# Kernel optimization log

Measured on AMD Instinct MI355X. Metric: run time of the kernel, lower is better.

Reference implementation:

```python
import jax, jax.numpy as jnp
import numpy as np

NU = 0.5

def _conv3x3(x, w):
    # x: [B,1,Hp,Wp] padded, w: [1,1,3,3]; VALID conv -> [B,1,H,W]
    return jax.lax.conv_general_dilated(
        x, w, window_strides=(1, 1), padding='VALID',
        dimension_numbers=('NCHW', 'OIHW', 'NCHW'))


def setup_inputs() -> dict:
    key = jax.random.key(0)
    k1, k2, k3, k4, k5 = jax.random.split(key, 5)
    B, H, W = 16, 1024, 1024
    u = jax.random.normal(k1, (B, 1, H, W), dtype=jnp.float32)
    u_vel = jax.random.normal(k2, (B, 1, H, W), dtype=jnp.float32)
    w1 = jax.random.normal(k3, (1, 1, 3, 3), dtype=jnp.float32)
    w2 = jax.random.normal(k4, (1, 1, 3, 3), dtype=jnp.float32)
    w3 = jax.random.normal(k5, (1, 1, 3, 3), dtype=jnp.float32)
    return {"u": u, "u_vel": u_vel, "w1": w1, "w2": w2, "w3": w3}


def reference(u, u_vel, w1, w2, w3):
    # replicate pad by 1 on H and W (torch 'replicate' == numpy 'edge')
    u_pad = jnp.pad(u, ((0, 0), (0, 0), (1, 1), (1, 1)), mode='edge')
    Lu = NU * _conv3x3(u_pad, w1) - u_vel * _conv3x3(u_pad, w2) - u_vel * _conv3x3(u_pad, w3)
    return Lu
```

## Files before the change

kernel.cpp:

```cpp
#include <hip/hip_runtime.h>


#define HH 1024
#define WW 1024
#define RPB 4
#define PPT 4
#define TPB (WW / PPT)

__device__ __forceinline__ float rfl(float x) {
    union { float f; int i; } c; c.f = x;
    c.i = __builtin_amdgcn_readfirstlane(c.i);
    return c.f;
}

__global__ __launch_bounds__(TPB) void burgers_stencil(
    const float* __restrict__ u,
    const float* __restrict__ uvel,
    const float* __restrict__ w1,
    const float* __restrict__ w2,
    const float* __restrict__ w3,
    float* __restrict__ out,
    int rowBlocks)
{
    const int tid = threadIdx.x;
    const int b   = blockIdx.x / rowBlocks;
    const int y0  = (blockIdx.x % rowBlocks) * RPB;
    const int x0  = tid * PPT;

    const size_t img = (size_t)b * HH * WW;
    const float* ub  = u + img;

    const int xl = (x0 == 0) ? 0 : x0 - 1;
    const int xr = (x0 + PPT >= WW) ? WW - 1 : x0 + PPT;

    float4 uv[RPB + 2]; float ul[RPB + 2], ur[RPB + 2];
#pragma unroll
    for (int i = 0; i < RPB + 2; ++i) {
        int yr = y0 - 1 + i;
        yr = yr < 0 ? 0 : (yr > HH - 1 ? HH - 1 : yr);
        const float* row = ub + (size_t)yr * WW;
        uv[i] = *(const float4*)(row + x0);
        ul[i] = row[xl];
        ur[i] = row[xr];
    }
    float4 vv[RPB];
#pragma unroll
    for (int r = 0; r < RPB; ++r)
        vv[r] = *(const float4*)(uvel + img + (size_t)(y0 + r) * WW + x0);

    float W1[9], W23[9];
#pragma unroll
    for (int i = 0; i < 9; ++i) {
        W1[i]  = rfl(w1[i]);
        W23[i] = rfl(w2[i] + w3[i]);
    }

    __builtin_amdgcn_sched_barrier(0);

#pragma unroll
    for (int r = 0; r < RPB; ++r) {
        float p[3][PPT + 2];
#pragma unroll
        for (int rr = 0; rr < 3; ++rr) {
            const int i = r + rr;
            p[rr][0] = ul[i];
            p[rr][1] = uv[i].x; p[rr][2] = uv[i].y;
            p[rr][3] = uv[i].z; p[rr][4] = uv[i].w;
            p[rr][5] = ur[i];
        }
        const float vel[PPT] = {vv[r].x, vv[r].y, vv[r].z, vv[r].w};

        float o[PPT];
#pragma unroll
        for (int j = 0; j < PPT; ++j) {
            float c1 = 0.f, c23 = 0.f;
#pragma unroll
            for (int rr = 0; rr < 3; ++rr) {
#pragma unroll
                for (int k = 0; k < 3; ++k) {
                    const float a = p[rr][j + k];
                    c1  = fmaf(W1[rr*3 + k],  a, c1);
                    c23 = fmaf(W23[rr*3 + k], a, c23);
                }
            }
            o[j] = 0.5f * c1 - vel[j] * c23;
        }
        float4 ov; ov.x = o[0]; ov.y = o[1]; ov.z = o[2]; ov.w = o[3];
        *(float4*)(out + img + (size_t)(y0 + r) * WW + x0) = ov;
    }
}

extern "C" void kernel_launch(void* const* d_in, const int* in_sizes, int n_in,
                              void* d_out, int out_size, void* d_ws, size_t ws_size,
                              hipStream_t stream) {
    const float* u    = (const float*)d_in[0];
    const float* uvel = (const float*)d_in[1];
    const float* w1   = (const float*)d_in[2];
    const float* w2   = (const float*)d_in[3];
    const float* w3   = (const float*)d_in[4];
    float* out        = (float*)d_out;

    const int B = in_sizes[0] / (HH * WW);
    const int rowBlocks = HH / RPB;
    dim3 grid(B * rowBlocks);
    dim3 block(TPB);
    burgers_stencil<<<grid, block, 0, stream>>>(u, uvel, w1, w2, w3, out, rowBlocks);
}
```

Measured before the change: 179.0 us.

## Stage stencil input rows into LDS via direct global-to-LDS loads

Measured after the change: 174.5 us. 1.03x faster.

```diff
diff --git a/kernel.cpp b/kernel.cpp
--- a/kernel.cpp
+++ b/kernel.cpp
@@ -4,8 +4,11 @@
 #define HH 1024
 #define WW 1024
 #define RPB 4
-#define PPT 4
-#define TPB (WW / PPT)
+#define TPB 256
+#define NROW (RPB + 2)
+
+typedef __attribute__((address_space(3))) void       lds_void;
+typedef __attribute__((address_space(1))) const void gbl_void;
 
 __device__ __forceinline__ float rfl(float x) {
     union { float f; int i; } c; c.f = x;
@@ -22,27 +25,28 @@
     float* __restrict__ out,
     int rowBlocks)
 {
-    const int tid = threadIdx.x;
-    const int b   = blockIdx.x / rowBlocks;
-    const int y0  = (blockIdx.x % rowBlocks) * RPB;
-    const int x0  = tid * PPT;
+    __shared__ float tile[NROW * WW];
+
+    const int tid  = threadIdx.x;
+    const int wave = tid >> 6;
+    const int lane = tid & 63;
+    const int b    = blockIdx.x / rowBlocks;
+    const int y0   = (blockIdx.x % rowBlocks) * RPB;
+    const int x0   = tid * 4;
 
     const size_t img = (size_t)b * HH * WW;
     const float* ub  = u + img;
 
-    const int xl = (x0 == 0) ? 0 : x0 - 1;
-    const int xr = (x0 + PPT >= WW) ? WW - 1 : x0 + PPT;
-
-    float4 uv[RPB + 2]; float ul[RPB + 2], ur[RPB + 2];
 #pragma unroll
-    for (int i = 0; i < RPB + 2; ++i) {
+    for (int i = 0; i < NROW; ++i) {
         int yr = y0 - 1 + i;
         yr = yr < 0 ? 0 : (yr > HH - 1 ? HH - 1 : yr);
-        const float* row = ub + (size_t)yr * WW;
-        uv[i] = *(const float4*)(row + x0);
-        ul[i] = row[xl];
-        ur[i] = row[xr];
+        const float* g = ub + (size_t)yr * WW + wave * 256 + lane * 4;
+        __builtin_amdgcn_global_load_lds((gbl_void*)g,
+                                         (lds_void*)&tile[i * WW + wave * 256],
+                                         16, 0, 0);
     }
+
     float4 vv[RPB];
 #pragma unroll
     for (int r = 0; r < RPB; ++r)
@@ -55,24 +59,28 @@
         W23[i] = rfl(w2[i] + w3[i]);
     }
 
-    __builtin_amdgcn_sched_barrier(0);
+    __syncthreads();
+
+    const int xm1 = (x0 == 0)       ? 0      : x0 - 1;
+    const int xp4 = (x0 + 4 >= WW)  ? WW - 1 : x0 + 4;
 
 #pragma unroll
     for (int r = 0; r < RPB; ++r) {
-        float p[3][PPT + 2];
+        float p[3][6];
 #pragma unroll
         for (int rr = 0; rr < 3; ++rr) {
-            const int i = r + rr;
-            p[rr][0] = ul[i];
-            p[rr][1] = uv[i].x; p[rr][2] = uv[i].y;
-            p[rr][3] = uv[i].z; p[rr][4] = uv[i].w;
-            p[rr][5] = ur[i];
+            const float* row = &tile[(r + rr) * WW];
+            const float4 m = *(const float4*)(row + x0);
+            p[rr][0] = row[xm1];
+            p[rr][1] = m.x; p[rr][2] = m.y;
+            p[rr][3] = m.z; p[rr][4] = m.w;
+            p[rr][5] = row[xp4];
         }
-        const float vel[PPT] = {vv[r].x, vv[r].y, vv[r].z, vv[r].w};
+        const float vel[4] = {vv[r].x, vv[r].y, vv[r].z, vv[r].w};
 
-        float o[PPT];
+        float o[4];
 #pragma unroll
-        for (int j = 0; j < PPT; ++j) {
+        for (int j = 0; j < 4; ++j) {
             float c1 = 0.f, c23 = 0.f;
 #pragma unroll
             for (int rr = 0; rr < 3; ++rr) {
```

## Use single-wave blocks covering 8 rows by 256 columns with waves-per-EU hint

Applied to the files above, without the earlier changes.

After: 174.3 us. -2.6%, faster.

```diff
diff --git a/kernel.cpp b/kernel.cpp
--- a/kernel.cpp
+++ b/kernel.cpp
@@ -3,9 +3,9 @@
 
 #define HH 1024
 #define WW 1024
-#define RPB 4
-#define PPT 4
-#define TPB (WW / PPT)
+#define RPB 8
+#define CPW 256
+#define NROW (RPB + 2)
 
 __device__ __forceinline__ float rfl(float x) {
     union { float f; int i; } c; c.f = x;
@@ -13,29 +13,42 @@
     return c.f;
 }
 
-__global__ __launch_bounds__(TPB) void burgers_stencil(
+__global__ __attribute__((amdgpu_flat_work_group_size(64, 64),
+                          amdgpu_waves_per_eu(1, 2)))
+void burgers_stencil(
     const float* __restrict__ u,
     const float* __restrict__ uvel,
     const float* __restrict__ w1,
     const float* __restrict__ w2,
     const float* __restrict__ w3,
     float* __restrict__ out,
-    int rowBlocks)
+    int rowBlocks, int colBlocks)
 {
-    const int tid = threadIdx.x;
-    const int b   = blockIdx.x / rowBlocks;
-    const int y0  = (blockIdx.x % rowBlocks) * RPB;
-    const int x0  = tid * PPT;
+    const int lane = threadIdx.x;
+    int rem = blockIdx.x;
+    const int xb = rem % colBlocks; rem /= colBlocks;
+    const int yb = rem % rowBlocks; rem /= rowBlocks;
+    const int b  = rem;
+
+    const int y0 = yb * RPB;
+    const int x0 = xb * CPW + lane * 4;
 
     const size_t img = (size_t)b * HH * WW;
     const float* ub  = u + img;
 
+    float W1[9], W23[9];
+#pragma unroll
+    for (int i = 0; i < 9; ++i) {
+        W1[i]  = rfl(w1[i]);
+        W23[i] = rfl(w2[i] + w3[i]);
+    }
+
     const int xl = (x0 == 0) ? 0 : x0 - 1;
-    const int xr = (x0 + PPT >= WW) ? WW - 1 : x0 + PPT;
+    const int xr = (x0 + 4 >= WW) ? WW - 1 : x0 + 4;
 
-    float4 uv[RPB + 2]; float ul[RPB + 2], ur[RPB + 2];
+    float4 uv[NROW]; float ul[NROW], ur[NROW];
 #pragma unroll
-    for (int i = 0; i < RPB + 2; ++i) {
+    for (int i = 0; i < NROW; ++i) {
         int yr = y0 - 1 + i;
         yr = yr < 0 ? 0 : (yr > HH - 1 ? HH - 1 : yr);
         const float* row = ub + (size_t)yr * WW;
@@ -48,18 +61,11 @@
     for (int r = 0; r < RPB; ++r)
         vv[r] = *(const float4*)(uvel + img + (size_t)(y0 + r) * WW + x0);
 
-    float W1[9], W23[9];
-#pragma unroll
-    for (int i = 0; i < 9; ++i) {
-        W1[i]  = rfl(w1[i]);
-        W23[i] = rfl(w2[i] + w3[i]);
-    }
-
     __builtin_amdgcn_sched_barrier(0);
 
 #pragma unroll
     for (int r = 0; r < RPB; ++r) {
-        float p[3][PPT + 2];
+        float p[3][6];
 #pragma unroll
         for (int rr = 0; rr < 3; ++rr) {
             const int i = r + rr;
@@ -68,11 +74,11 @@
             p[rr][3] = uv[i].z; p[rr][4] = uv[i].w;
             p[rr][5] = ur[i];
         }
-        const float vel[PPT] = {vv[r].x, vv[r].y, vv[r].z, vv[r].w};
+        const float vel[4] = {vv[r].x, vv[r].y, vv[r].z, vv[r].w};
 
-        float o[PPT];
+        float o[4];
 #pragma unroll
-        for (int j = 0; j < PPT; ++j) {
+        for (int j = 0; j < 4; ++j) {
             float c1 = 0.f, c23 = 0.f;
 #pragma unroll
             for (int rr = 0; rr < 3; ++rr) {
@@ -83,7 +89,7 @@
                     c23 = fmaf(W23[rr*3 + k], a, c23);
                 }
             }
-            o[j] = 0.5f * c1 - vel[j] * c23;
+            o[j] = fmaf(-vel[j], c23, 0.5f * c1);
         }
         float4 ov; ov.x = o[0]; ov.y = o[1]; ov.z = o[2]; ov.w = o[3];
         *(float4*)(out + img + (size_t)(y0 + r) * WW + x0) = ov;
@@ -102,7 +108,9 @@
 
     const int B = in_sizes[0] / (HH * WW);
     const int rowBlocks = HH / RPB;
-    dim3 grid(B * rowBlocks);
-    dim3 block(TPB);
-    burgers_stencil<<<grid, block, 0, stream>>>(u, uvel, w1, w2, w3, out, rowBlocks);
+    const int colBlocks = WW / CPW;
+    dim3 grid(B * rowBlocks * colBlocks);
+    dim3 block(64);
+    burgers_stencil<<<grid, block, 0, stream>>>(u, uvel, w1, w2, w3, out,
+                                                rowBlocks, colBlocks);
 }
```
